# Optimization experiments

Measured on AMD Instinct MI355X. Metric: run time of the kernel, lower is better.

Reference implementation:

```python
import jax, jax.numpy as jnp
import numpy as np

TRAIN_COUNT, FEAT = 20000, 40
BATCH, NN, M = 2048, 64, 10


def _safe_l2(d2):
    # sqrt with zero (not NaN/inf) gradient at d2 == 0 (diagonal of pairwise dists)
    pos = d2 > 0
    return jnp.where(pos, jnp.sqrt(jnp.where(pos, d2, 1.0)), 0.0)


def setup_inputs() -> dict:
    key = jax.random.key(0)
    k1, k2, k3, k4 = jax.random.split(key, 4)
    x = jax.random.normal(k1, (TRAIN_COUNT, FEAT), dtype=jnp.float32)
    batch_indices = jax.random.randint(k2, (BATCH,), 0, TRAIN_COUNT)
    batch_nn_indices = jax.random.randint(k3, (BATCH, NN), 0, TRAIN_COUNT)
    batch_nn_targets = jax.random.normal(k4, (BATCH, NN, M), dtype=jnp.float32)
    length_scale = jnp.ones((M,), dtype=jnp.float32)
    eps = 1e-3 * jnp.ones((M,), dtype=jnp.float32)
    return {
        "x": x,
        "length_scale": length_scale,
        "eps": eps,
        "batch_indices": batch_indices,
        "batch_nn_indices": batch_nn_indices,
        "batch_nn_targets": batch_nn_targets,
    }


def reference(x, length_scale, eps, batch_indices, batch_nn_indices, batch_nn_targets):
    b, nn, m = batch_nn_targets.shape
    xb = x[batch_indices]          # (b, f)
    xn = x[batch_nn_indices]       # (b, nn, f)

    # crosswise l2 distances (b, nn)
    cd = _safe_l2(jnp.sum((xb[:, None, :] - xn) ** 2, axis=-1))
    # pairwise l2 distances (b, nn, nn)
    pd = _safe_l2(jnp.sum((xn[:, :, None, :] - xn[:, None, :, :]) ** 2, axis=-1))

    # Matern nu = 1/2: k(d) = exp(-d / length_scale); vectorized over the m models
    Kcross = jnp.exp(-cd[None, :, :] / length_scale[:, None, None])            # (m, b, nn)
    K = jnp.exp(-pd[None, :, :, :] / length_scale[:, None, None, None])        # (m, b, nn, nn)
    eye = jnp.eye(nn, dtype=K.dtype)
    Kp = K + eps[:, None, None, None] * eye                                     # homoscedastic perturb

    Y = jnp.moveaxis(batch_nn_targets, -1, 0)[..., None]                        # (m, b, nn, 1)
    F = jnp.linalg.solve(Kp, Y)[..., 0]                                         # (m, b, nn)
    predictions = jnp.einsum("mbn,mbn->bm", Kcross, F)

    G = jnp.linalg.solve(Kp, Kcross[..., None])[..., 0]                         # (m, b, nn)
    variances = 1.0 - jnp.einsum("mbn,mbn->bm", Kcross, G)

    sigma_sq = jnp.sum(Y[..., 0] * F, axis=(1, 2)) / (b * nn)                   # (m,)
    return predictions, variances, sigma_sq
```

## Files before the change

### kernel.cpp

```cpp
#include <hip/hip_runtime.h>
#include <math.h>

#define BATCH 2048
#define NN 64
#define FEAT 40
#define M 10
#define ASZ (NN * NN + 64)

typedef float v2f __attribute__((ext_vector_type(2)));

#define PKFMA_SV(acc, s_src, v_src) \
    asm("v_pk_fma_f32 %0, %1, %2, %0" : "+v"(acc) : "s"(s_src), "v"(v_src))
#define PKFMA_VV(acc, a_src, b_src) \
    asm("v_pk_fma_f32 %0, %1, %2, %0" : "+v"(acc) : "v"(a_src), "v"(b_src))

__device__ __forceinline__ float rl(float v, int l) {
    return __int_as_float(__builtin_amdgcn_readlane(__float_as_int(v), l));
}
__device__ __forceinline__ int rli(int v, int l) {
    return __builtin_amdgcn_readlane(v, l);
}
__device__ __forceinline__ float wsum(float v) {
#pragma unroll
    for (int o = 32; o >= 1; o >>= 1) v += __shfl_xor(v, o, 64);
    return v;
}

__global__ __launch_bounds__(64)
__attribute__((amdgpu_waves_per_eu(2, 2)))
void muygps_kernel(
    const float* __restrict__ x,
    const float* __restrict__ ls,
    const float* __restrict__ epsv,
    const int*   __restrict__ bidx,
    const int*   __restrict__ nidx,
    const float* __restrict__ tgt,
    float* __restrict__ out,
    float* __restrict__ ws)
{
    __shared__ float A[ASZ];
    __shared__ float rvb[NN];

    const int b    = blockIdx.x;
    const int lane = threadIdx.x;

    const int nv = nidx[b * NN + lane];
    const float* xr0 = x + (size_t)nv * FEAT;
    v2f xc2[FEAT / 2];
#pragma unroll
    for (int q = 0; q < FEAT / 4; ++q) {
        const float4 v = *(const float4*)(xr0 + 4 * q);
        xc2[2 * q]     = v2f{v.x, v.y};
        xc2[2 * q + 1] = v2f{v.z, v.w};
    }
    v2f nl2 = {0.f, 0.f};
#pragma unroll
    for (int q = 0; q < FEAT / 2; ++q) PKFMA_VV(nl2, xc2[q], xc2[q]);
    const float nl = nl2.x + nl2.y;

    const v2f* xbv = (const v2f*)(x + (size_t)bidx[b] * FEAT);
    v2f gc2 = {0.f, 0.f}, nb2 = {0.f, 0.f};
#pragma unroll
    for (int q = 0; q < FEAT / 2; ++q) {
        const v2f xbq = xbv[q];
        PKFMA_VV(gc2, xbq, xc2[q]);
        PKFMA_VV(nb2, xbq, xbq);
    }
    float cd2 = ((nb2.x + nb2.y) + nl) - 2.f * (gc2.x + gc2.y);
    cd2 = (cd2 < 0.05f) ? 0.f : cd2;
    const float cdv = sqrtf(cd2);

    unsigned done = 0;
    const unsigned all = (1u << M) - 1u;
    while (true) {
        const int   lead = __ffs(~done) - 1;
        const float lls  = ls[lead];
        const float lep  = epsv[lead];
        const float il   = -1.0f / lls;

#pragma unroll 2
        for (int i = 0; i < NN; i += 2) {
            const int ri0 = rli(nv, i), ri1 = rli(nv, i + 1);
            const v2f* rp0 = (const v2f*)(x + (size_t)ri0 * FEAT);
            const v2f* rp1 = (const v2f*)(x + (size_t)ri1 * FEAT);
            v2f g0 = {0.f, 0.f}, g1 = {0.f, 0.f};
#pragma unroll
            for (int q = 0; q < FEAT / 2; ++q) {
                const v2f r0q = rp0[q], r1q = rp1[q];
                PKFMA_SV(g0, r0q, xc2[q]);
                PKFMA_SV(g1, r1q, xc2[q]);
            }
            const float ga = g0.x + g0.y, gb = g1.x + g1.y;
            float d2a = (rl(ga, i) + nl) - 2.f * ga;
            float d2b = (rl(gb, i + 1) + nl) - 2.f * gb;
            d2a = (d2a < 0.05f) ? 0.f : d2a;
            d2b = (d2b < 0.05f) ? 0.f : d2b;
            float va = __expf(sqrtf(d2a) * il);
            float vb = __expf(sqrtf(d2b) * il);
            if (lane == i)     va += lep;
            if (lane == i + 1) vb += lep;
            A[i * NN + lane]       = va;
            A[(i + 1) * NN + lane] = vb;
        }
        const float kcv = __expf(cdv * il);

        float z[M + 1];
        z[0] = kcv;
        {
            const float* trow = tgt + ((size_t)b * NN + lane) * M;
#pragma unroll
            for (int q = 0; q < M / 2; ++q) {
                const float2 v = *(const float2*)(trow + 2 * q);
                z[2 * q + 1] = v.x; z[2 * q + 2] = v.y;
            }
        }

        float pc0 = A[lane];
        float pc1 = A[NN + lane];
        for (int p = 0; p < 31; ++p) {
            const int k = 2 * p;
            const float d0  = rl(pc0, k);
            const float r0  = __builtin_amdgcn_rcpf(d0);
            const float cv0 = pc0 * (-r0);
            pc1 = fmaf(cv0, rl(pc0, k + 1), pc1);
            const float d1  = rl(pc1, k + 1);
            const float r1  = __builtin_amdgcn_rcpf(d1);
            const float cv1 = pc1 * (-r1);
            A[k * NN + lane]      = (lane > k)     ? pc0 * r0 : 0.f;
            A[k * NN + NN + lane] = (lane > k + 1) ? pc1 * r1 : 0.f;
            rvb[k]     = r0;
            rvb[k + 1] = r1;
            float t2 = A[(k + 2) * NN + lane];
            float t3 = A[(k + 3) * NN + lane];
            float u0 = 0.f, u1 = 0.f;
            if (k + 4 < NN) { u0 = A[(k + 4) * NN + lane]; u1 = A[(k + 5) * NN + lane]; }
            t2 = fmaf(cv0, rl(pc0, k + 2), t2); t2 = fmaf(cv1, rl(pc1, k + 2), t2);
            t3 = fmaf(cv0, rl(pc0, k + 3), t3); t3 = fmaf(cv1, rl(pc1, k + 3), t3);
            for (int i = k + 4; i < NN; i += 2) {
                float a0 = u0, a1 = u1;
                if (i + 2 < NN) {
                    u0 = A[(i + 2) * NN + lane];
                    u1 = A[(i + 3) * NN + lane];
                }
                a0 = fmaf(cv0, rl(pc0, i), a0);     a0 = fmaf(cv1, rl(pc1, i), a0);
                a1 = fmaf(cv0, rl(pc0, i + 1), a1); a1 = fmaf(cv1, rl(pc1, i + 1), a1);
                A[i * NN + lane]       = a0;
                A[(i + 1) * NN + lane] = a1;
            }
            pc0 = t2; pc1 = t3;
        }
        {
            const float d0  = rl(pc0, 62);
            const float r0  = __builtin_amdgcn_rcpf(d0);
            const float cv0 = pc0 * (-r0);
            pc1 = fmaf(cv0, rl(pc0, 63), pc1);
            const float d1  = rl(pc1, 63);
            const float r1  = __builtin_amdgcn_rcpf(d1);
            A[62 * NN + lane] = (lane > 62) ? pc0 * r0 : 0.f;
            rvb[62] = r0;
            rvb[63] = r1;
        }

        float lr = A[lane];
        for (int k = 0; k < NN - 1; ++k) {
            const float lrn = A[(k + 1) * NN + lane];
            const float lv = -lr;
#pragma unroll
            for (int j = 0; j < M + 1; ++j) {
                const float s = rl(z[j], k);
                z[j] = fmaf(lv, s, z[j]);
            }
            lr = lrn;
        }

        const float rvv = rvb[lane];
        const float zc  = z[0];
        const float quad = wsum(zc * zc * rvv);
        unsigned mb = 0;
#pragma unroll
        for (int m = 0; m < M; ++m)
            if (!(done & (1u << m)) && ls[m] == lls && epsv[m] == lep)
                mb |= 1u << m;
        float predv = 0.f, sigv = 0.f;
#pragma unroll
        for (int m = 0; m < M; ++m) {
            if (mb & (1u << m)) {
                const float zm = z[m + 1];
                const float pm = wsum(zc * zm * rvv);
                const float sm = wsum(zm * zm * rvv);
                if (lane == m) { predv = pm; sigv = sm; }
            }
        }
        if (lane < M && ((mb >> lane) & 1u)) {
            out[b * M + lane] = predv;
            out[BATCH * M + b * M + lane] = 1.0f - quad;
            ws[lane * BATCH + b] = sigv;
        }
        done |= mb;
        if (done == all) break;
    }
}

__global__ __launch_bounds__(640)
void sigma_reduce(const float* __restrict__ ws, float* __restrict__ out) {
    const int w = threadIdx.x >> 6, lane = threadIdx.x & 63;
    const float4* p = (const float4*)(ws + w * BATCH);
    float a = 0.f;
#pragma unroll
    for (int i = 0; i < BATCH / 4 / 64; ++i) {
        const float4 v = p[i * 64 + lane];
        a += (v.x + v.y) + (v.z + v.w);
    }
    a = wsum(a);
    if (lane == 0)
        out[2 * BATCH * M + w] = a * (1.0f / (float)(BATCH * NN));
}

extern "C" void kernel_launch(void* const* d_in, const int* in_sizes, int n_in,
                              void* d_out, int out_size, void* d_ws, size_t ws_size,
                              hipStream_t stream) {
    const float* x   = (const float*)d_in[0];
    const float* lsp = (const float*)d_in[1];
    const float* ep  = (const float*)d_in[2];
    const int*   bi  = (const int*)d_in[3];
    const int*   ni  = (const int*)d_in[4];
    const float* tg  = (const float*)d_in[5];
    float* out = (float*)d_out;
    float* ws  = (float*)d_ws;

    muygps_kernel<<<BATCH, 64, 0, stream>>>(x, lsp, ep, bi, ni, tg, out, ws);
    sigma_reduce<<<1, 640, 0, stream>>>(ws, out);
}
```

Baseline: 156.6 us.

## Fuse forward substitution into LDL factorization and deepen LDS prefetch

The forward elimination of the right-hand sides (the kcross and target vectors) now happens inside each factorization step using the current pivot multipliers. This removes the separate forward-substitution pass and the stores of the normalized L rows to LDS. The row loads from LDS are also prefetched two row-pairs ahead, and the shared buffer is padded so those out-of-range loads stay in bounds. The cost is more live registers and more readlanes interleaved within each pivot step.

After: 147.0 us. -6.2%, faster.

```diff
diff --git a/kernel.cpp b/kernel.cpp
--- a/kernel.cpp
+++ b/kernel.cpp
@@ -5,7 +5,7 @@
 #define NN 64
 #define FEAT 40
 #define M 10
-#define ASZ (NN * NN + 64)
+#define ASZ (68 * NN)
 
 typedef float v2f __attribute__((ext_vector_type(2)));
 
@@ -117,8 +117,14 @@
 
         float pc0 = A[lane];
         float pc1 = A[NN + lane];
+        float n2  = A[2 * NN + lane];
+        float n3  = A[3 * NN + lane];
         for (int p = 0; p < 31; ++p) {
             const int k = 2 * p;
+            float v0 = A[(k + 4) * NN + lane];
+            float v1 = A[(k + 5) * NN + lane];
+            float u0 = A[(k + 6) * NN + lane];
+            float u1 = A[(k + 7) * NN + lane];
             const float d0  = rl(pc0, k);
             const float r0  = __builtin_amdgcn_rcpf(d0);
             const float cv0 = pc0 * (-r0);
@@ -126,22 +132,24 @@
             const float d1  = rl(pc1, k + 1);
             const float r1  = __builtin_amdgcn_rcpf(d1);
             const float cv1 = pc1 * (-r1);
-            A[k * NN + lane]      = (lane > k)     ? pc0 * r0 : 0.f;
-            A[k * NN + NN + lane] = (lane > k + 1) ? pc1 * r1 : 0.f;
             rvb[k]     = r0;
             rvb[k + 1] = r1;
-            float t2 = A[(k + 2) * NN + lane];
-            float t3 = A[(k + 3) * NN + lane];
-            float u0 = 0.f, u1 = 0.f;
-            if (k + 4 < NN) { u0 = A[(k + 4) * NN + lane]; u1 = A[(k + 5) * NN + lane]; }
-            t2 = fmaf(cv0, rl(pc0, k + 2), t2); t2 = fmaf(cv1, rl(pc1, k + 2), t2);
-            t3 = fmaf(cv0, rl(pc0, k + 3), t3); t3 = fmaf(cv1, rl(pc1, k + 3), t3);
-            for (int i = k + 4; i < NN; i += 2) {
+            const float lv0 = (lane > k)     ? cv0 : 0.f;
+            const float lv1 = (lane > k + 1) ? cv1 : 0.f;
+#pragma unroll
+            for (int j = 0; j < M + 1; ++j) {
+                z[j] = fmaf(lv0, rl(z[j], k), z[j]);
+                z[j] = fmaf(lv1, rl(z[j], k + 1), z[j]);
+            }
+            const float t2 = fmaf(cv1, rl(pc1, k + 2), fmaf(cv0, rl(pc0, k + 2), n2));
+            const float t3 = fmaf(cv1, rl(pc1, k + 3), fmaf(cv0, rl(pc0, k + 3), n3));
+            v0 = fmaf(cv0, rl(pc0, k + 4), v0); v0 = fmaf(cv1, rl(pc1, k + 4), v0);
+            v1 = fmaf(cv0, rl(pc0, k + 5), v1); v1 = fmaf(cv1, rl(pc1, k + 5), v1);
+            n2 = v0; n3 = v1;
+            for (int i = k + 6; i < NN; i += 2) {
                 float a0 = u0, a1 = u1;
-                if (i + 2 < NN) {
-                    u0 = A[(i + 2) * NN + lane];
-                    u1 = A[(i + 3) * NN + lane];
-                }
+                u0 = A[(i + 2) * NN + lane];
+                u1 = A[(i + 3) * NN + lane];
                 a0 = fmaf(cv0, rl(pc0, i), a0);     a0 = fmaf(cv1, rl(pc1, i), a0);
                 a1 = fmaf(cv0, rl(pc0, i + 1), a1); a1 = fmaf(cv1, rl(pc1, i + 1), a1);
                 A[i * NN + lane]       = a0;
@@ -156,21 +164,12 @@
             pc1 = fmaf(cv0, rl(pc0, 63), pc1);
             const float d1  = rl(pc1, 63);
             const float r1  = __builtin_amdgcn_rcpf(d1);
-            A[62 * NN + lane] = (lane > 62) ? pc0 * r0 : 0.f;
             rvb[62] = r0;
             rvb[63] = r1;
-        }
-
-        float lr = A[lane];
-        for (int k = 0; k < NN - 1; ++k) {
-            const float lrn = A[(k + 1) * NN + lane];
-            const float lv = -lr;
-#pragma unroll
-            for (int j = 0; j < M + 1; ++j) {
-                const float s = rl(z[j], k);
-                z[j] = fmaf(lv, s, z[j]);
-            }
-            lr = lrn;
+            const float lv0 = (lane > 62) ? cv0 : 0.f;
+#pragma unroll
+            for (int j = 0; j < M + 1; ++j)
+                z[j] = fmaf(lv0, rl(z[j], 62), z[j]);
         }
 
         const float rvv = rvb[lane];
```
